# Performance work log

Measured on AMD Instinct MI355X. Metric: run time of the kernel, lower is better.

## Reference

```python
import jax, jax.numpy as jnp
import numpy as np

N = 16384
IN_DIM = 128
OUT_DIM = 128
NUM_TYPES = 8


def setup_inputs() -> dict:
    key = jax.random.key(0)
    k1, k2, k3, k4 = jax.random.split(key, 4)
    x = jax.random.normal(k1, (N, IN_DIM), dtype=jnp.float32)
    node_types = jax.random.randint(k2, (N,), 0, NUM_TYPES, dtype=jnp.int32)
    adjacency = jax.random.uniform(k3, (N, N), dtype=jnp.float32)
    weight = jax.random.normal(k4, (NUM_TYPES, OUT_DIM, IN_DIM), dtype=jnp.float32)
    return {"x": x, "node_types": node_types, "adjacency": adjacency, "weight": weight}


def reference(x, node_types, adjacency, weight):
    # agg = A @ x : (N, in_dim)
    agg = jnp.matmul(adjacency, x)
    # Per-type projection: compute agg @ W[t].T for all types, then select
    # by node type. (N, T, out) intermediate is small (N*T*out floats).
    per_type = jnp.einsum("nd,tod->nto", agg, weight)  # (N, T, out)
    out = jnp.take_along_axis(per_type, node_types[:, None, None].astype(jnp.int32), axis=1)
    return out[:, 0, :]  # (N, out)
```

## Files before the change

kernel.cpp:

```cpp
#include <hip/hip_runtime.h>
#include <stdint.h>


#define N_NODES 16384
#define DIM     128
#define NTYPES  8
#define BM      64
#define BK      128
#define NT_K    (N_NODES / BK)

typedef float  f32x4  __attribute__((ext_vector_type(4)));
typedef __bf16 bf16x4 __attribute__((ext_vector_type(4)));
typedef __bf16 bf16x8 __attribute__((ext_vector_type(8)));

__device__ __attribute__((aligned(16))) unsigned short g_xT[DIM * N_NODES];
__device__ __attribute__((aligned(16))) unsigned short g_Wb[NTYPES * DIM * DIM];

__device__ __forceinline__ unsigned int f2b(float f) {
    unsigned int u = __float_as_uint(f);
    u += 0x7FFFu + ((u >> 16) & 1u);
    return u >> 16;
}
#define BF_LO(u) __uint_as_float((unsigned int)(u) << 16)
#define BF_HI(u) __uint_as_float((unsigned int)(u) & 0xFFFF0000u)

__device__ __forceinline__ bf16x4 cvt4(const f32x4 v) {
    bf16x4 r;
    r[0] = (__bf16)v[0]; r[1] = (__bf16)v[1]; r[2] = (__bf16)v[2]; r[3] = (__bf16)v[3];
    return r;
}


__global__ void prep_all(const float* __restrict__ x, const float* __restrict__ w) {
    const int tid = threadIdx.x;
    if (blockIdx.x < 64) {
        int n = blockIdx.x * 256 + tid;
        const float* row = x + (size_t)n * DIM;
#pragma unroll
        for (int d0 = 0; d0 < DIM; d0 += 4) {
            float4 v = *(const float4*)(row + d0);
            g_xT[(d0 + 0) * N_NODES + n] = (unsigned short)f2b(v.x);
            g_xT[(d0 + 1) * N_NODES + n] = (unsigned short)f2b(v.y);
            g_xT[(d0 + 2) * N_NODES + n] = (unsigned short)f2b(v.z);
            g_xT[(d0 + 3) * N_NODES + n] = (unsigned short)f2b(v.w);
        }
    } else {
        int base = ((blockIdx.x - 64) * 256 + tid) * 16;
#pragma unroll
        for (int j = 0; j < 4; ++j) {
            float4 v = *(const float4*)(w + base + j * 4);
            ushort4 o;
            o.x = (unsigned short)f2b(v.x); o.y = (unsigned short)f2b(v.y);
            o.z = (unsigned short)f2b(v.z); o.w = (unsigned short)f2b(v.w);
            *(ushort4*)(g_Wb + base + j * 4) = o;
        }
    }
}


#define AB_BYTES 16384
#define XB_BYTES 32768

#define GLOAD16(g, l) __builtin_amdgcn_global_load_lds(                         \
    (const __attribute__((address_space(1))) unsigned int*)(g),                 \
    (__attribute__((address_space(3))) unsigned int*)(l), 16, 0, 0)

#define ALOADI(reg, ptr) \
    asm volatile("global_load_dwordx4 %0, %1, off" : "=v"(reg) : "v"(ptr))

#define ISSUE_AL(R0, R1, R2, R3) do {            \
    ALOADI(R0, pA0); ALOADI(R1, pA1);            \
    ALOADI(R2, pA2); ALOADI(R3, pA3);            \
    pA0 += BK; pA1 += BK; pA2 += BK; pA3 += BK;  \
} while (0)

#define ISSUE_XD(Xb) do {                        \
    GLOAD16(gX0, (Xb) + 0 * 8192 + wq);          \
    GLOAD16(gX1, (Xb) + 1 * 8192 + wq);          \
    GLOAD16(gX2, (Xb) + 2 * 8192 + wq);          \
    GLOAD16(gX3, (Xb) + 3 * 8192 + wq);          \
    gX0 += BK; gX1 += BK; gX2 += BK; gX3 += BK;  \
} while (0)

#define STOREA(As, R0, R1, R2, R3) do {          \
    *(bf16x4*)((As) + aw0) = cvt4(R0);           \
    *(bf16x4*)((As) + aw1) = cvt4(R1);           \
    *(bf16x4*)((As) + aw2) = cvt4(R2);           \
    *(bf16x4*)((As) + aw3) = cvt4(R3);           \
} while (0)

#define KS(Ab, Xb, off) do {                                                    \
    bf16x8 a0_ = *(const bf16x8*)((Ab) + arA0 + (off));                         \
    bf16x8 a1_ = *(const bf16x8*)((Ab) + arA1 + (off));                         \
    bf16x8 b0_ = *(const bf16x8*)((Xb) + xB0 + (off));                          \
    bf16x8 b1_ = *(const bf16x8*)((Xb) + xB1 + (off));                          \
    acc00 = __builtin_amdgcn_mfma_f32_16x16x32_bf16(a0_, b0_, acc00, 0, 0, 0);  \
    acc01 = __builtin_amdgcn_mfma_f32_16x16x32_bf16(a0_, b1_, acc01, 0, 0, 0);  \
    acc10 = __builtin_amdgcn_mfma_f32_16x16x32_bf16(a1_, b0_, acc10, 0, 0, 0);  \
    acc11 = __builtin_amdgcn_mfma_f32_16x16x32_bf16(a1_, b1_, acc11, 0, 0, 0);  \
} while (0)

#define COMPUTE(Ab, Xb) do {      \
    KS(Ab, Xb, off0);             \
    KS(Ab, Xb, off1);             \
    KS(Ab, Xb, off2);             \
    KS(Ab, Xb, off3);             \
} while (0)

#define WAITV(N) do {                                        \
    asm volatile("s_waitcnt vmcnt(" #N ")" ::: "memory");    \
    __builtin_amdgcn_sched_barrier(0);                       \
} while (0)

#define TOP(VM) do {                                                            \
    asm volatile("s_waitcnt vmcnt(" #VM ") lgkmcnt(0)\n\ts_barrier" ::: "memory"); \
    __builtin_amdgcn_sched_barrier(0);                                          \
} while (0)

#define PHASE(Ac, Xc, As, S0,S1,S2,S3, L0,L1,L2,L3, Xi) do {  \
    TOP(8);                                                   \
    COMPUTE(Ac, Xc);                                          \
    __builtin_amdgcn_sched_barrier(0);                        \
    WAITV(4);                                                 \
    STOREA(As, S0, S1, S2, S3);                               \
    ISSUE_AL(L0, L1, L2, L3);                                 \
    ISSUE_XD(Xi);                                             \
} while (0)

__global__ __launch_bounds__(512, 1) void gconv_main(
    const float* __restrict__ adj,
    const int* __restrict__ types,
    float* __restrict__ out)
{
    __shared__ __align__(16) unsigned char lds[3 * XB_BYTES + 2 * AB_BYTES];
    unsigned char* X0 = lds;
    unsigned char* X1 = lds + XB_BYTES;
    unsigned char* X2 = lds + 2 * XB_BYTES;
    unsigned char* Ab0 = lds + 3 * XB_BYTES;
    unsigned char* Ab1 = Ab0 + AB_BYTES;

    const int tid  = threadIdx.x;
    const int w    = tid >> 6;
    const int l    = tid & 63;
    const int m0   = blockIdx.x * BM;

    const int mrow = (w & 1) * 32;
    const int ncol = (w >> 1) * 32;
    const int h    = l >> 4;

    f32x4 acc00 = {}, acc01 = {}, acc10 = {}, acc11 = {};

    const int rj0 = w * 8 + 0 + (l >> 5);
    const int rj1 = w * 8 + 2 + (l >> 5);
    const int rj2 = w * 8 + 4 + (l >> 5);
    const int rj3 = w * 8 + 6 + (l >> 5);
    const float* pA0 = adj + (size_t)(m0 + rj0) * N_NODES + (l & 31) * 4;
    const float* pA1 = adj + (size_t)(m0 + rj1) * N_NODES + (l & 31) * 4;
    const float* pA2 = adj + (size_t)(m0 + rj2) * N_NODES + (l & 31) * 4;
    const float* pA3 = adj + (size_t)(m0 + rj3) * N_NODES + (l & 31) * 4;
    const int g_   = l & 31;
    const int aw0 = rj0 * 256 + ((((g_ >> 1) ^ (rj0 & 7))) << 4) + ((g_ & 1) << 3);
    const int aw1 = rj1 * 256 + ((((g_ >> 1) ^ (rj1 & 7))) << 4) + ((g_ & 1) << 3);
    const int aw2 = rj2 * 256 + ((((g_ >> 1) ^ (rj2 & 7))) << 4) + ((g_ & 1) << 3);
    const int aw3 = rj3 * 256 + ((((g_ >> 1) ^ (rj3 & 7))) << 4) + ((g_ & 1) << 3);

    const int xdw = 4 * w + (l >> 4);
    const unsigned short* gX0 = g_xT + (size_t)( 0 + xdw) * N_NODES + (((l & 15) ^ (xdw & 7)) << 3);
    const unsigned short* gX1 = g_xT + (size_t)(32 + xdw) * N_NODES + (((l & 15) ^ (xdw & 7)) << 3);
    const unsigned short* gX2 = g_xT + (size_t)(64 + xdw) * N_NODES + (((l & 15) ^ (xdw & 7)) << 3);
    const unsigned short* gX3 = g_xT + (size_t)(96 + xdw) * N_NODES + (((l & 15) ^ (xdw & 7)) << 3);
    const int wq = w << 10;

    const int arA0 = (mrow +  0 + (l & 15)) * 256;
    const int arA1 = (mrow + 16 + (l & 15)) * 256;
    const int xB0  = (ncol +  0 + (l & 15)) * 256;
    const int xB1  = (ncol + 16 + (l & 15)) * 256;
    const int off0 = (( 0 + h) ^ (l & 7)) << 4;
    const int off1 = (( 4 + h) ^ (l & 7)) << 4;
    const int off2 = (( 8 + h) ^ (l & 7)) << 4;
    const int off3 = ((12 + h) ^ (l & 7)) << 4;

    f32x4 p0, p1, p2, p3, q0, q1, q2, q3;

    ISSUE_AL(p0, p1, p2, p3);
    ISSUE_XD(X0);
    ISSUE_AL(q0, q1, q2, q3);
    ISSUE_XD(X1);
    WAITV(12);
    STOREA(Ab0, p0, p1, p2, p3);

    for (int i = 0; i < 21; ++i) {
        PHASE(Ab0, X0, Ab1, q0,q1,q2,q3, p0,p1,p2,p3, X2);
        PHASE(Ab1, X1, Ab0, p0,p1,p2,p3, q0,q1,q2,q3, X0);
        PHASE(Ab0, X2, Ab1, q0,q1,q2,q3, p0,p1,p2,p3, X1);
        PHASE(Ab1, X0, Ab0, p0,p1,p2,p3, q0,q1,q2,q3, X2);
        PHASE(Ab0, X1, Ab1, q0,q1,q2,q3, p0,p1,p2,p3, X0);
        PHASE(Ab1, X2, Ab0, p0,p1,p2,p3, q0,q1,q2,q3, X1);
    }
    TOP(8);
    COMPUTE(Ab0, X0);
    __builtin_amdgcn_sched_barrier(0);
    WAITV(4);
    STOREA(Ab1, q0, q1, q2, q3);
    TOP(0);
    COMPUTE(Ab1, X1);
    __syncthreads();

    float* agg = (float*)lds;
#pragma unroll
    for (int r = 0; r < 4; ++r) {
        const int r0 = (mrow +  0 + h * 4 + r) * 132 + ncol + (l & 15);
        const int r1 = (mrow + 16 + h * 4 + r) * 132 + ncol + (l & 15);
        agg[r0 +  0] = acc00[r];
        agg[r0 + 16] = acc01[r];
        agg[r1 +  0] = acc10[r];
        agg[r1 + 16] = acc11[r];
    }
    __syncthreads();

    const int rbase = w * 8;
    for (int rr = 0; rr < 8; ++rr) {
        const int rw = rbase + rr;
        const int nn = m0 + rw;
        const int ty = types[nn];
        const unsigned short* Wt = g_Wb + ty * (DIM * DIM);
        const int o0 = l * 2;
        const float* aggRow = agg + rw * 132;
        float s0 = 0.f, s1 = 0.f;
#pragma unroll
        for (int d0 = 0; d0 < DIM; d0 += 8) {
            float4 ga = *(const float4*)(aggRow + d0);
            float4 gb = *(const float4*)(aggRow + d0 + 4);
            uint4 wa = *(const uint4*)(Wt + o0 * DIM + d0);
            uint4 wb = *(const uint4*)(Wt + (o0 + 1) * DIM + d0);
            s0 += ga.x * BF_LO(wa.x) + ga.y * BF_HI(wa.x) + ga.z * BF_LO(wa.y) + ga.w * BF_HI(wa.y);
            s0 += gb.x * BF_LO(wa.z) + gb.y * BF_HI(wa.z) + gb.z * BF_LO(wa.w) + gb.w * BF_HI(wa.w);
            s1 += ga.x * BF_LO(wb.x) + ga.y * BF_HI(wb.x) + ga.z * BF_LO(wb.y) + ga.w * BF_HI(wb.y);
            s1 += gb.x * BF_LO(wb.z) + gb.y * BF_HI(wb.z) + gb.z * BF_LO(wb.w) + gb.w * BF_HI(wb.w);
        }
        float2 res; res.x = s0; res.y = s1;
        *(float2*)(out + (size_t)nn * DIM + o0) = res;
    }
}


extern "C" void kernel_launch(void* const* d_in, const int* in_sizes, int n_in,
                              void* d_out, int out_size, void* d_ws, size_t ws_size,
                              hipStream_t stream) {
    const float* x     = (const float*)d_in[0];
    const int*   types = (const int*)d_in[1];
    const float* adj   = (const float*)d_in[2];
    const float* wt    = (const float*)d_in[3];
    float* out = (float*)d_out;

    hipLaunchKernelGGL(prep_all, dim3(96), dim3(256), 0, stream, x, wt);
    hipLaunchKernelGGL(gconv_main, dim3(N_NODES / BM), dim3(512), 0, stream, adj, types, out);
}
```

Before: 302.5 us.

## Load two adjacency K-tiles per issue with immediate offsets, restructure pipeline phases

The adjacency load pattern changes from one 128-column tile per phase to two consecutive tiles every other phase, using immediate instruction offsets to fetch both from one pointer. The main loop becomes alternating odd and even phases with retuned vmcnt waits, and the prologue and epilogue are rewritten to match. The aim is to cut address arithmetic, issue longer contiguous row reads, and give A loads more time in flight before they are needed. In exchange, half the phases issue no A loads, so memory traffic is burstier, and the hand-tuned wait counts must stay correct.

Result: faster. 289.5 us (-4.3%).

```diff
diff --git a/kernel.cpp b/kernel.cpp
--- a/kernel.cpp
+++ b/kernel.cpp
@@ -65,13 +65,15 @@
     (const __attribute__((address_space(1))) unsigned int*)(g),                 \
     (__attribute__((address_space(3))) unsigned int*)(l), 16, 0, 0)
 
-#define ALOADI(reg, ptr) \
-    asm volatile("global_load_dwordx4 %0, %1, off" : "=v"(reg) : "v"(ptr))
-
-#define ISSUE_AL(R0, R1, R2, R3) do {            \
-    ALOADI(R0, pA0); ALOADI(R1, pA1);            \
-    ALOADI(R2, pA2); ALOADI(R3, pA3);            \
-    pA0 += BK; pA1 += BK; pA2 += BK; pA3 += BK;  \
+#define ALOADI(reg, ptr, off) \
+    asm volatile("global_load_dwordx4 %0, %1, off offset:" #off : "=v"(reg) : "v"(ptr))
+
+#define ISSUE_AL2() do {                          \
+    ALOADI(p0, pA0, 0); ALOADI(q0, pA0, 512);     \
+    ALOADI(p1, pA1, 0); ALOADI(q1, pA1, 512);     \
+    ALOADI(p2, pA2, 0); ALOADI(q2, pA2, 512);     \
+    ALOADI(p3, pA3, 0); ALOADI(q3, pA3, 512);     \
+    pA0 += 256; pA1 += 256; pA2 += 256; pA3 += 256; \
 } while (0)
 
 #define ISSUE_XD(Xb) do {                        \
@@ -117,14 +119,20 @@
     __builtin_amdgcn_sched_barrier(0);                                          \
 } while (0)
 
-#define PHASE(Ac, Xc, As, S0,S1,S2,S3, L0,L1,L2,L3, Xi) do {  \
-    TOP(8);                                                   \
-    COMPUTE(Ac, Xc);                                          \
-    __builtin_amdgcn_sched_barrier(0);                        \
-    WAITV(4);                                                 \
-    STOREA(As, S0, S1, S2, S3);                               \
-    ISSUE_AL(L0, L1, L2, L3);                                 \
-    ISSUE_XD(Xi);                                             \
+#define PH_ODD(Xc, Xi) do {                      \
+    TOP(12);                                     \
+    COMPUTE(Ab1, Xc);                            \
+    WAITV(5);                                    \
+    STOREA(Ab0, p0, p1, p2, p3);                 \
+    ISSUE_XD(Xi);                                \
+} while (0)
+
+#define PH_EVEN(Xc, Xi) do {                     \
+    TOP(4);                                      \
+    COMPUTE(Ab0, Xc);                            \
+    STOREA(Ab1, q0, q1, q2, q3);                 \
+    ISSUE_AL2();                                 \
+    ISSUE_XD(Xi);                                \
 } while (0)
 
 __global__ __launch_bounds__(512, 1) void gconv_main(
@@ -158,7 +166,7 @@
     const float* pA1 = adj + (size_t)(m0 + rj1) * N_NODES + (l & 31) * 4;
     const float* pA2 = adj + (size_t)(m0 + rj2) * N_NODES + (l & 31) * 4;
     const float* pA3 = adj + (size_t)(m0 + rj3) * N_NODES + (l & 31) * 4;
-    const int g_   = l & 31;
+    const int g_  = l & 31;
     const int aw0 = rj0 * 256 + ((((g_ >> 1) ^ (rj0 & 7))) << 4) + ((g_ & 1) << 3);
     const int aw1 = rj1 * 256 + ((((g_ >> 1) ^ (rj1 & 7))) << 4) + ((g_ & 1) << 3);
     const int aw2 = rj2 * 256 + ((((g_ >> 1) ^ (rj2 & 7))) << 4) + ((g_ & 1) << 3);
@@ -182,25 +190,32 @@
 
     f32x4 p0, p1, p2, p3, q0, q1, q2, q3;
 
-    ISSUE_AL(p0, p1, p2, p3);
+    ISSUE_AL2();
     ISSUE_XD(X0);
-    ISSUE_AL(q0, q1, q2, q3);
     ISSUE_XD(X1);
-    WAITV(12);
+    WAITV(9);
     STOREA(Ab0, p0, p1, p2, p3);
-
-    for (int i = 0; i < 21; ++i) {
-        PHASE(Ab0, X0, Ab1, q0,q1,q2,q3, p0,p1,p2,p3, X2);
-        PHASE(Ab1, X1, Ab0, p0,p1,p2,p3, q0,q1,q2,q3, X0);
-        PHASE(Ab0, X2, Ab1, q0,q1,q2,q3, p0,p1,p2,p3, X1);
-        PHASE(Ab1, X0, Ab0, p0,p1,p2,p3, q0,q1,q2,q3, X2);
-        PHASE(Ab0, X1, Ab1, q0,q1,q2,q3, p0,p1,p2,p3, X0);
-        PHASE(Ab1, X2, Ab0, p0,p1,p2,p3, q0,q1,q2,q3, X1);
-    }
-    TOP(8);
+    TOP(4);
     COMPUTE(Ab0, X0);
-    __builtin_amdgcn_sched_barrier(0);
-    WAITV(4);
+    STOREA(Ab1, q0, q1, q2, q3);
+    ISSUE_AL2();
+    ISSUE_XD(X2);
+
+    for (int i = 0; i < 20; ++i) {
+        PH_ODD (X1, X0);
+        PH_EVEN(X2, X1);
+        PH_ODD (X0, X2);
+        PH_EVEN(X1, X0);
+        PH_ODD (X2, X1);
+        PH_EVEN(X0, X2);
+    }
+    PH_ODD (X1, X0);
+    PH_EVEN(X2, X1);
+    PH_ODD (X0, X2);
+    PH_EVEN(X1, X0);
+    PH_ODD (X2, X1);
+    TOP(4);
+    COMPUTE(Ab0, X0);
     STOREA(Ab1, q0, q1, q2, q3);
     TOP(0);
     COMPUTE(Ab1, X1);
```

## Batch adjacency loads four K-tiles at a time with immediate offsets

Applied to the files above, without the earlier changes.

Restructures the main loop so that each wave issues 16 adjacency loads, covering four consecutive K-tiles through the instruction's immediate offsets, once every four phases instead of four loads every phase. Those registers are then drained into the LDS A buffers over the following phases. The goal is a deeper prefetch of the dominant adjacency stream and fewer address increments. The cost is 16 extra VGPRs of staging and a more complex vmcnt schedule. The phase count still totals 128 K-tiles, and the other renames are cosmetic.

New measurement: 285.8 us. 1.06x faster.

```diff
diff --git a/kernel.cpp b/kernel.cpp
--- a/kernel.cpp
+++ b/kernel.cpp
@@ -65,13 +65,15 @@
     (const __attribute__((address_space(1))) unsigned int*)(g),                 \
     (__attribute__((address_space(3))) unsigned int*)(l), 16, 0, 0)
 
-#define ALOADI(reg, ptr) \
-    asm volatile("global_load_dwordx4 %0, %1, off" : "=v"(reg) : "v"(ptr))
-
-#define ISSUE_AL(R0, R1, R2, R3) do {            \
-    ALOADI(R0, pA0); ALOADI(R1, pA1);            \
-    ALOADI(R2, pA2); ALOADI(R3, pA3);            \
-    pA0 += BK; pA1 += BK; pA2 += BK; pA3 += BK;  \
+#define ALOADI(reg, ptr, off) \
+    asm volatile("global_load_dwordx4 %0, %1, off offset:" #off : "=v"(reg) : "v"(ptr))
+
+#define ISSUE_AL4() do {                                                   \
+    ALOADI(p0, pA0, 0); ALOADI(q0, pA0, 512); ALOADI(r0, pA0, 1024); ALOADI(s0, pA0, 1536); \
+    ALOADI(p1, pA1, 0); ALOADI(q1, pA1, 512); ALOADI(r1, pA1, 1024); ALOADI(s1, pA1, 1536); \
+    ALOADI(p2, pA2, 0); ALOADI(q2, pA2, 512); ALOADI(r2, pA2, 1024); ALOADI(s2, pA2, 1536); \
+    ALOADI(p3, pA3, 0); ALOADI(q3, pA3, 512); ALOADI(r3, pA3, 1024); ALOADI(s3, pA3, 1536); \
+    pA0 += 512; pA1 += 512; pA2 += 512; pA3 += 512;                        \
 } while (0)
 
 #define ISSUE_XD(Xb) do {                        \
@@ -117,15 +119,10 @@
     __builtin_amdgcn_sched_barrier(0);                                          \
 } while (0)
 
-#define PHASE(Ac, Xc, As, S0,S1,S2,S3, L0,L1,L2,L3, Xi) do {  \
-    TOP(8);                                                   \
-    COMPUTE(Ac, Xc);                                          \
-    __builtin_amdgcn_sched_barrier(0);                        \
-    WAITV(4);                                                 \
-    STOREA(As, S0, S1, S2, S3);                               \
-    ISSUE_AL(L0, L1, L2, L3);                                 \
-    ISSUE_XD(Xi);                                             \
-} while (0)
+#define PH_A0(Xc, Xi) do { TOP(4);  COMPUTE(Ab0, Xc); STOREA(Ab1, q0,q1,q2,q3); ISSUE_XD(Xi); } while (0)
+#define PH_A1(Xc, Xi) do { TOP(4);  COMPUTE(Ab1, Xc); STOREA(Ab0, r0,r1,r2,r3); ISSUE_XD(Xi); } while (0)
+#define PH_A2(Xc, Xi) do { TOP(4);  COMPUTE(Ab0, Xc); STOREA(Ab1, s0,s1,s2,s3); ISSUE_AL4(); ISSUE_XD(Xi); } while (0)
+#define PH_A3(Xc, Xi) do { TOP(20); COMPUTE(Ab1, Xc); WAITV(7); STOREA(Ab0, p0,p1,p2,p3); ISSUE_XD(Xi); } while (0)
 
 __global__ __launch_bounds__(512, 1) void gconv_main(
     const float* __restrict__ adj,
@@ -158,7 +155,7 @@
     const float* pA1 = adj + (size_t)(m0 + rj1) * N_NODES + (l & 31) * 4;
     const float* pA2 = adj + (size_t)(m0 + rj2) * N_NODES + (l & 31) * 4;
     const float* pA3 = adj + (size_t)(m0 + rj3) * N_NODES + (l & 31) * 4;
-    const int g_   = l & 31;
+    const int g_  = l & 31;
     const int aw0 = rj0 * 256 + ((((g_ >> 1) ^ (rj0 & 7))) << 4) + ((g_ & 1) << 3);
     const int aw1 = rj1 * 256 + ((((g_ >> 1) ^ (rj1 & 7))) << 4) + ((g_ & 1) << 3);
     const int aw2 = rj2 * 256 + ((((g_ >> 1) ^ (rj2 & 7))) << 4) + ((g_ & 1) << 3);
@@ -180,41 +177,45 @@
     const int off2 = (( 8 + h) ^ (l & 7)) << 4;
     const int off3 = ((12 + h) ^ (l & 7)) << 4;
 
-    f32x4 p0, p1, p2, p3, q0, q1, q2, q3;
-
-    ISSUE_AL(p0, p1, p2, p3);
+    f32x4 p0, p1, p2, p3, q0, q1, q2, q3,
+          r0, r1, r2, r3, s0, s1, s2, s3;
+
+    ISSUE_AL4();
     ISSUE_XD(X0);
-    ISSUE_AL(q0, q1, q2, q3);
     ISSUE_XD(X1);
-    WAITV(12);
+    WAITV(8);
     STOREA(Ab0, p0, p1, p2, p3);
 
-    for (int i = 0; i < 21; ++i) {
-        PHASE(Ab0, X0, Ab1, q0,q1,q2,q3, p0,p1,p2,p3, X2);
-        PHASE(Ab1, X1, Ab0, p0,p1,p2,p3, q0,q1,q2,q3, X0);
-        PHASE(Ab0, X2, Ab1, q0,q1,q2,q3, p0,p1,p2,p3, X1);
-        PHASE(Ab1, X0, Ab0, p0,p1,p2,p3, q0,q1,q2,q3, X2);
-        PHASE(Ab0, X1, Ab1, q0,q1,q2,q3, p0,p1,p2,p3, X0);
-        PHASE(Ab1, X2, Ab0, p0,p1,p2,p3, q0,q1,q2,q3, X1);
-    }
-    TOP(8);
+    for (int i = 0; i < 10; ++i) {
+        PH_A0(X0, X2); PH_A1(X1, X0); PH_A2(X2, X1); PH_A3(X0, X2);
+        PH_A0(X1, X0); PH_A1(X2, X1); PH_A2(X0, X2); PH_A3(X1, X0);
+        PH_A0(X2, X1); PH_A1(X0, X2); PH_A2(X1, X0); PH_A3(X2, X1);
+    }
+    PH_A0(X0, X2); PH_A1(X1, X0); PH_A2(X2, X1); PH_A3(X0, X2);
+    TOP(4);
+    COMPUTE(Ab0, X1);
+    STOREA(Ab1, q0, q1, q2, q3);
+    ISSUE_XD(X0);
+    TOP(4);
+    COMPUTE(Ab1, X2);
+    STOREA(Ab0, r0, r1, r2, r3);
+    ISSUE_XD(X1);
+    TOP(4);
     COMPUTE(Ab0, X0);
-    __builtin_amdgcn_sched_barrier(0);
-    WAITV(4);
-    STOREA(Ab1, q0, q1, q2, q3);
+    STOREA(Ab1, s0, s1, s2, s3);
     TOP(0);
     COMPUTE(Ab1, X1);
     __syncthreads();
 
     float* agg = (float*)lds;
 #pragma unroll
-    for (int r = 0; r < 4; ++r) {
-        const int r0 = (mrow +  0 + h * 4 + r) * 132 + ncol + (l & 15);
-        const int r1 = (mrow + 16 + h * 4 + r) * 132 + ncol + (l & 15);
-        agg[r0 +  0] = acc00[r];
-        agg[r0 + 16] = acc01[r];
-        agg[r1 +  0] = acc10[r];
-        agg[r1 + 16] = acc11[r];
+    for (int rr = 0; rr < 4; ++rr) {
+        const int e0 = (mrow +  0 + h * 4 + rr) * 132 + ncol + (l & 15);
+        const int e1 = (mrow + 16 + h * 4 + rr) * 132 + ncol + (l & 15);
+        agg[e0 +  0] = acc00[rr];
+        agg[e0 + 16] = acc01[rr];
+        agg[e1 +  0] = acc10[rr];
+        agg[e1 + 16] = acc11[rr];
     }
     __syncthreads();
 
@@ -226,19 +227,19 @@
         const unsigned short* Wt = g_Wb + ty * (DIM * DIM);
         const int o0 = l * 2;
         const float* aggRow = agg + rw * 132;
-        float s0 = 0.f, s1 = 0.f;
+        float t0 = 0.f, t1 = 0.f;
 #pragma unroll
         for (int d0 = 0; d0 < DIM; d0 += 8) {
             float4 ga = *(const float4*)(aggRow + d0);
             float4 gb = *(const float4*)(aggRow + d0 + 4);
             uint4 wa = *(const uint4*)(Wt + o0 * DIM + d0);
             uint4 wb = *(const uint4*)(Wt + (o0 + 1) * DIM + d0);
-            s0 += ga.x * BF_LO(wa.x) + ga.y * BF_HI(wa.x) + ga.z * BF_LO(wa.y) + ga.w * BF_HI(wa.y);
-            s0 += gb.x * BF_LO(wa.z) + gb.y * BF_HI(wa.z) + gb.z * BF_LO(wa.w) + gb.w * BF_HI(wa.w);
-            s1 += ga.x * BF_LO(wb.x) + ga.y * BF_HI(wb.x) + ga.z * BF_LO(wb.y) + ga.w * BF_HI(wb.y);
-            s1 += gb.x * BF_LO(wb.z) + gb.y * BF_HI(wb.z) + gb.z * BF_LO(wb.w) + gb.w * BF_HI(wb.w);
+            t0 += ga.x * BF_LO(wa.x) + ga.y * BF_HI(wa.x) + ga.z * BF_LO(wa.y) + ga.w * BF_HI(wa.y);
+            t0 += gb.x * BF_LO(wa.z) + gb.y * BF_HI(wa.z) + gb.z * BF_LO(wa.w) + gb.w * BF_HI(wa.w);
+            t1 += ga.x * BF_LO(wb.x) + ga.y * BF_HI(wb.x) + ga.z * BF_LO(wb.y) + ga.w * BF_HI(wb.y);
+            t1 += gb.x * BF_LO(wb.z) + gb.y * BF_HI(wb.z) + gb.z * BF_LO(wb.w) + gb.w * BF_HI(wb.w);
         }
-        float2 res; res.x = s0; res.y = s1;
+        float2 res; res.x = t0; res.y = t1;
         *(float2*)(out + (size_t)nn * DIM + o0) = res;
     }
 }
```
